# Performance work log

Hardware: AMD Instinct MI355X
Metric: run time of the kernel (lower is better)

The kernel has to match this reference:

```python
import jax, jax.numpy as jnp
import numpy as np

N_HEAD = 12
D_MODEL = 768
D_K = 64
D_V = 64
ALPHA = 1.0
DIST_SCALE = 1.0
TEMPERATURE = D_K ** 0.5
LN_EPS = 1e-6
EPS = 1e-12

B = 16
SEQ = 577  # 1 CLS + 24*24 patches


def setup_inputs() -> dict:
    key = jax.random.key(0)
    ks = jax.random.split(key, 10)
    s = 1.0 / np.sqrt(D_MODEL)
    return {
        "q": jax.random.normal(ks[0], (B, SEQ, D_MODEL), jnp.float32),
        "k": jax.random.normal(ks[1], (B, SEQ, D_MODEL), jnp.float32),
        "v": jax.random.normal(ks[2], (B, SEQ, D_MODEL), jnp.float32),
        "patch_positions": jax.random.uniform(ks[3], (B, SEQ - 1, 2), jnp.float32) * 24.0,
        "patch_embeddings": jax.random.normal(ks[4], (B, SEQ, D_MODEL), jnp.float32),
        # weights stored as (in, out): y = x @ W
        "w_qs": jax.random.normal(ks[5], (D_MODEL, N_HEAD * D_K), jnp.float32) * s,
        "w_ks": jax.random.normal(ks[6], (D_MODEL, N_HEAD * D_K), jnp.float32) * s,
        "w_vs": jax.random.normal(ks[7], (D_MODEL, N_HEAD * D_V), jnp.float32) * s,
        "w_fc": jax.random.normal(ks[8], (N_HEAD * D_V, D_MODEL), jnp.float32) * s,
        "ln_gamma": jnp.ones((D_MODEL,), jnp.float32),
        "ln_beta": jnp.zeros((D_MODEL,), jnp.float32),
    }


def _shape_bias_penalty(pos, emb, alpha, dist_scale):
    # pos: (B, P, 2) patch coordinates; emb: (B, P, E) patch embeddings (no CLS)
    # penalty[b,i,j] = alpha * cos_sim(e_i, e_j) * dist_scale * ||p_i - p_j||
    diff = pos[:, :, None, :] - pos[:, None, :, :]          # (B, P, P, 2)
    dist = jnp.sqrt(jnp.sum(diff * diff, axis=-1) + EPS)    # (B, P, P)
    e = emb * jax.lax.rsqrt(jnp.sum(emb * emb, axis=-1, keepdims=True) + EPS)
    sim = jnp.einsum("bie,bje->bij", e, e)                  # (B, P, P)
    return alpha * sim * (dist_scale * dist)


def reference(q, k, v, patch_positions, patch_embeddings,
              w_qs, w_ks, w_vs, w_fc, ln_gamma, ln_beta):
    b, n, _ = q.shape
    residual = q
    # project and split heads: (B, H, N, Dh)
    qh = (q @ w_qs).reshape(b, n, N_HEAD, D_K).transpose(0, 2, 1, 3)
    kh = (k @ w_ks).reshape(b, n, N_HEAD, D_K).transpose(0, 2, 1, 3)
    vh = (v @ w_vs).reshape(b, n, N_HEAD, D_V).transpose(0, 2, 1, 3)

    logits = jnp.einsum("bhid,bhjd->bhij", qh / TEMPERATURE, kh)  # (B, H, N, N)
    penalty = _shape_bias_penalty(patch_positions, patch_embeddings[:, 1:, :],
                                  ALPHA, DIST_SCALE)              # (B, P, P)
    logits = logits.at[:, :, 1:, 1:].add(-penalty[:, None, :, :])

    attn = jax.nn.softmax(logits, axis=-1)
    out = jnp.einsum("bhij,bhjd->bhid", attn, vh)                 # (B, H, N, Dv)
    out = out.transpose(0, 2, 1, 3).reshape(b, n, N_HEAD * D_V)
    out = out @ w_fc + residual

    mu = jnp.mean(out, axis=-1, keepdims=True)
    var = jnp.mean((out - mu) ** 2, axis=-1, keepdims=True)
    return (out - mu) * jax.lax.rsqrt(var + LN_EPS) * ln_gamma + ln_beta
```

## Files before the change

### kernel.cpp

```cpp
#include <hip/hip_runtime.h>
#include <hip/hip_bf16.h>

#define B_   16
#define SEQ  577
#define P_   576
#define DM   768
#define NH   12
#define DK   64
#define TEMP 8.0f
#define LNEPS 1e-6f
#define EPS_  1e-12f
#define MROWS (B_*SEQ)

typedef __attribute__((ext_vector_type(8))) short short8;
typedef __attribute__((ext_vector_type(4))) float f32x4;

static const size_t PEN_B = 0;
static const size_t QH_B  = 21233664;
static const size_t KH_B  = 35414016;
static const size_t VH_B  = 49594368;
static const size_t VT_B  = 63774720;
static const size_t OBF_B = 79503360;
static const size_t WT_B  = 93683712;
static const size_t RN_B  = 98402304;
static const size_t FC_B  = QH_B;

__device__ __forceinline__ bool bf_flag(const void* gamma) {
    return (((const unsigned int*)gamma)[0] & 0xFFFFu) != 0u;
}
__device__ __forceinline__ float ldf(const void* p, size_t i, bool bf) {
    if (bf) {
        unsigned int w = ((unsigned int)((const unsigned short*)p)[i]) << 16;
        return __uint_as_float(w);
    }
    return ((const float*)p)[i];
}
__device__ __forceinline__ unsigned short f2bu(float x) {
    __hip_bfloat16 h = __float2bfloat16(x);
    return *(unsigned short*)&h;
}

__device__ __forceinline__ int xcd_chunk(int orig, int nwg) {
    int q = nwg >> 3, r = nwg & 7;
    int xcd = orig & 7, slot = orig >> 3;
    int base = xcd < r ? xcd * (q + 1) : r * (q + 1) + (xcd - r) * q;
    return base + slot;
}

__global__ __launch_bounds__(256) void k_rownorm(const void* __restrict__ emb,
                                                 const void* __restrict__ gamma,
                                                 float* __restrict__ rn) {
    bool bf = bf_flag(gamma);
    int row = blockIdx.x;
    int b = row / P_, i = row % P_;
    size_t base = ((size_t)(b * SEQ + 1 + i)) * DM;
    float s = 0.f;
    for (int c = threadIdx.x; c < DM; c += 256) { float v = ldf(emb, base + c, bf); s += v * v; }
    __shared__ float red[4];
    for (int off = 32; off > 0; off >>= 1) s += __shfl_down(s, off, 64);
    int lane = threadIdx.x & 63, w = threadIdx.x >> 6;
    if (lane == 0) red[w] = s;
    __syncthreads();
    if (threadIdx.x == 0) rn[row] = rsqrtf(red[0] + red[1] + red[2] + red[3] + EPS_);
}

__global__ __launch_bounds__(256) void k_wt(const void* __restrict__ w0,
                                            const void* __restrict__ w1,
                                            const void* __restrict__ w2,
                                            const void* __restrict__ w3,
                                            const void* __restrict__ gamma,
                                            unsigned short* __restrict__ wt) {
    bool bf = bf_flag(gamma);
    int which = blockIdx.z;
    const void* W = which == 0 ? w0 : (which == 1 ? w1 : (which == 2 ? w2 : w3));
    unsigned short* WT = wt + (size_t)which * DM * DM;
    int k0 = blockIdx.y * 64, n0 = blockIdx.x * 64;
    __shared__ unsigned short Ts[64][69];
    int tid = threadIdx.x;
    {
        int kr = tid >> 2, nq = (tid & 3) * 16;
        size_t src = (size_t)(k0 + kr) * DM + n0 + nq;
        #pragma unroll
        for (int u = 0; u < 16; u++) Ts[kr][nq + u] = f2bu(ldf(W, src + u, bf));
    }
    __syncthreads();
    {
        int nr = tid >> 2, kq = (tid & 3) * 16;
        unsigned short tmp[16];
        #pragma unroll
        for (int u = 0; u < 16; u++) tmp[u] = Ts[kq + u][nr];
        uint4* dst = (uint4*)(WT + (size_t)(n0 + nr) * DM + k0 + kq);
        dst[0] = *(const uint4*)&tmp[0];
        dst[1] = *(const uint4*)&tmp[8];
    }
}

__global__ __launch_bounds__(256) void k_penalty_mfma(const void* __restrict__ emb,
                                                      const void* __restrict__ pos,
                                                      const void* __restrict__ gamma,
                                                      const float* __restrict__ rn,
                                                      float* __restrict__ pen) {
    bool bf = bf_flag(gamma);
    int p = xcd_chunk(blockIdx.x, 9 * 9 * B_);
    int b = p / 81; int rem = p % 81;
    int i0 = (rem / 9) * 64, j0 = (rem % 9) * 64;
    __shared__ __align__(16) unsigned short As[64][72];
    __shared__ __align__(16) unsigned short Bs[64][72];
    int tid = threadIdx.x;
    int lane = tid & 63, w = tid >> 6;

    f32x4 acc[4];
    #pragma unroll
    for (int c = 0; c < 4; c++) acc[c] = (f32x4){0.f, 0.f, 0.f, 0.f};

    int srow = tid >> 2, sq = (tid & 3) * 16;
    size_t ebase = ((size_t)b * SEQ + 1) * DM;
    size_t sa = ebase + (size_t)(i0 + srow) * DM + sq;
    size_t sb = ebase + (size_t)(j0 + srow) * DM + sq;

    for (int kc = 0; kc < DM; kc += 64) {
        if (bf) {
            const uint4* pa = (const uint4*)((const unsigned short*)emb + sa + kc);
            const uint4* pb = (const uint4*)((const unsigned short*)emb + sb + kc);
            *(uint4*)&As[srow][sq] = pa[0]; *(uint4*)&As[srow][sq + 8] = pa[1];
            *(uint4*)&Bs[srow][sq] = pb[0]; *(uint4*)&Bs[srow][sq + 8] = pb[1];
        } else {
            const float* pa = (const float*)emb + sa + kc;
            const float* pb = (const float*)emb + sb + kc;
            unsigned short ta[16], tb[16];
            #pragma unroll
            for (int u = 0; u < 4; u++) {
                float4 fa = ((const float4*)pa)[u];
                float4 fb = ((const float4*)pb)[u];
                ta[u*4+0] = f2bu(fa.x); ta[u*4+1] = f2bu(fa.y);
                ta[u*4+2] = f2bu(fa.z); ta[u*4+3] = f2bu(fa.w);
                tb[u*4+0] = f2bu(fb.x); tb[u*4+1] = f2bu(fb.y);
                tb[u*4+2] = f2bu(fb.z); tb[u*4+3] = f2bu(fb.w);
            }
            *(uint4*)&As[srow][sq] = *(const uint4*)&ta[0];
            *(uint4*)&As[srow][sq + 8] = *(const uint4*)&ta[8];
            *(uint4*)&Bs[srow][sq] = *(const uint4*)&tb[0];
            *(uint4*)&Bs[srow][sq + 8] = *(const uint4*)&tb[8];
        }
        __syncthreads();
        #pragma unroll
        for (int s = 0; s < 2; s++) {
            short8 af = *(const short8*)&As[w * 16 + (lane & 15)][s * 32 + (lane >> 4) * 8];
            #pragma unroll
            for (int c = 0; c < 4; c++) {
                short8 bfr = *(const short8*)&Bs[c * 16 + (lane & 15)][s * 32 + (lane >> 4) * 8];
                acc[c] = __builtin_amdgcn_mfma_f32_16x16x32_bf16(af, bfr, acc[c], 0, 0, 0);
            }
        }
        __syncthreads();
    }
    size_t pbase = (size_t)b * P_ * 2;
    int rbase = (lane >> 4) * 4, cbase = lane & 15;
    float pix[4], piy[4], rni_[4], pjx[4], pjy[4], rnj_[4];
    #pragma unroll
    for (int jj = 0; jj < 4; jj++) {
        int i = i0 + w * 16 + rbase + jj;
        pix[jj] = ldf(pos, pbase + (size_t)i * 2, bf);
        piy[jj] = ldf(pos, pbase + (size_t)i * 2 + 1, bf);
        rni_[jj] = rn[b * P_ + i];
    }
    #pragma unroll
    for (int c = 0; c < 4; c++) {
        int j = j0 + c * 16 + cbase;
        pjx[c] = ldf(pos, pbase + (size_t)j * 2, bf);
        pjy[c] = ldf(pos, pbase + (size_t)j * 2 + 1, bf);
        rnj_[c] = rn[b * P_ + j];
    }
    float* pp = pen + (size_t)b * P_ * P_;
    #pragma unroll
    for (int c = 0; c < 4; c++)
        #pragma unroll
        for (int jj = 0; jj < 4; jj++) {
            int i = i0 + w * 16 + rbase + jj;
            int j = j0 + c * 16 + cbase;
            float dx = pix[jj] - pjx[c], dy = piy[jj] - pjy[c];
            pp[(size_t)i * P_ + j] = acc[c][jj] * rni_[jj] * rnj_[c] * sqrtf(dx * dx + dy * dy + EPS_);
        }
}

__global__ __launch_bounds__(256) void k_proj_mfma(const void* __restrict__ q,
                                                   const void* __restrict__ k,
                                                   const void* __restrict__ v,
                                                   const unsigned short* __restrict__ wt,
                                                   const void* __restrict__ gamma,
                                                   unsigned short* __restrict__ qh,
                                                   unsigned short* __restrict__ kh,
                                                   unsigned short* __restrict__ vh) {
    bool bf = bf_flag(gamma);
    int p = xcd_chunk(blockIdx.x, 73 * 6 * 3);
    int which = p / (73 * 6);
    int rem = p % (73 * 6);
    int m0 = (rem / 6) * 128, n0 = (rem % 6) * 128;
    const void* X = which == 0 ? q : (which == 1 ? k : v);
    const unsigned short* WT = wt + (size_t)which * DM * DM;
    unsigned short* Y = which == 0 ? qh : (which == 1 ? kh : vh);
    float scale = which == 0 ? (1.0f / TEMP) : 1.0f;

    __shared__ __align__(16) unsigned short As[128][72];
    __shared__ __align__(16) unsigned short Bs[128][72];
    int tid = threadIdx.x;
    int lane = tid & 63, w = tid >> 6;
    int wr = w >> 1, wc = w & 1;

    f32x4 acc[4][4];
    #pragma unroll
    for (int r = 0; r < 4; r++)
        #pragma unroll
        for (int c = 0; c < 4; c++) acc[r][c] = (f32x4){0.f, 0.f, 0.f, 0.f};

    int sr = tid >> 1, sh = (tid & 1) * 32;
    int gm_s = m0 + sr; if (gm_s >= MROWS) gm_s = MROWS - 1;
    const size_t arow = (size_t)gm_s * DM;
    const size_t brow = (size_t)(n0 + sr) * DM;

    for (int kc = 0; kc < DM; kc += 64) {
        if (bf) {
            const uint4* src = (const uint4*)((const unsigned short*)X + arow + kc + sh);
            #pragma unroll
            for (int u = 0; u < 4; u++) *(uint4*)&As[sr][sh + u * 8] = src[u];
        } else {
            const float* src = (const float*)X + arow + kc + sh;
            unsigned short tmp[32];
            #pragma unroll
            for (int u = 0; u < 8; u++) {
                float4 f = ((const float4*)src)[u];
                tmp[u*4+0] = f2bu(f.x); tmp[u*4+1] = f2bu(f.y);
                tmp[u*4+2] = f2bu(f.z); tmp[u*4+3] = f2bu(f.w);
            }
            #pragma unroll
            for (int u = 0; u < 4; u++) *(uint4*)&As[sr][sh + u * 8] = *(const uint4*)&tmp[u * 8];
        }
        {
            const uint4* src = (const uint4*)(WT + brow + kc + sh);
            #pragma unroll
            for (int u = 0; u < 4; u++) *(uint4*)&Bs[sr][sh + u * 8] = src[u];
        }
        __syncthreads();
        #pragma unroll
        for (int s = 0; s < 2; s++) {
            short8 af[4], bfr[4];
            #pragma unroll
            for (int r = 0; r < 4; r++)
                af[r] = *(const short8*)&As[wr * 64 + r * 16 + (lane & 15)][s * 32 + (lane >> 4) * 8];
            #pragma unroll
            for (int c = 0; c < 4; c++)
                bfr[c] = *(const short8*)&Bs[wc * 64 + c * 16 + (lane & 15)][s * 32 + (lane >> 4) * 8];
            #pragma unroll
            for (int r = 0; r < 4; r++)
                #pragma unroll
                for (int c = 0; c < 4; c++)
                    acc[r][c] = __builtin_amdgcn_mfma_f32_16x16x32_bf16(af[r], bfr[c], acc[r][c], 0, 0, 0);
        }
        __syncthreads();
    }
    int rbase = (lane >> 4) * 4, cbase = lane & 15;
    #pragma unroll
    for (int r = 0; r < 4; r++) {
        #pragma unroll
        for (int jj = 0; jj < 4; jj++) {
            int gm = m0 + wr * 64 + r * 16 + rbase + jj;
            if (gm < MROWS) {
                int b = gm / SEQ, n = gm % SEQ;
                #pragma unroll
                for (int c = 0; c < 4; c++) {
                    int gc = n0 + wc * 64 + c * 16 + cbase;
                    int h = gc >> 6, d = gc & 63;
                    Y[(((size_t)(b * NH + h) * SEQ) + n) * DK + d] = f2bu(acc[r][c][jj] * scale);
                }
            }
        }
    }
}

__global__ __launch_bounds__(256) void k_vt(const unsigned short* __restrict__ vh,
                                            unsigned short* __restrict__ vt) {
    int ntile = blockIdx.x;
    int bh = blockIdx.y;
    __shared__ unsigned short Ts[64][72];
    int tid = threadIdx.x;
    int n0 = ntile * 64;
    {
        int r = tid >> 2, c = (tid & 3) * 16;
        int gn = n0 + r; if (gn > 576) gn = 576;
        const uint4* src = (const uint4*)(vh + ((size_t)bh * SEQ + gn) * DK + c);
        uint4 a = src[0], bv = src[1];
        *(uint4*)&Ts[r][c] = a; *(uint4*)&Ts[r][c + 8] = bv;
    }
    __syncthreads();
    {
        int d = tid >> 2, c = (tid & 3) * 16;
        unsigned short tmp[16];
        #pragma unroll
        for (int u = 0; u < 16; u++) tmp[u] = Ts[c + u][d];
        uint4* dst = (uint4*)(vt + ((size_t)bh * DK + d) * 640 + n0 + c);
        dst[0] = *(uint4*)&tmp[0];
        dst[1] = *(uint4*)&tmp[8];
    }
}

__global__ __launch_bounds__(512, 4) void k_attn2(const unsigned short* __restrict__ qh,
                                                  const unsigned short* __restrict__ kh,
                                                  const unsigned short* __restrict__ vt,
                                                  const float* __restrict__ pen,
                                                  unsigned short* __restrict__ O) {
    const int NWG = 5 * NH * B_;
    int flat = blockIdx.x + 5 * (blockIdx.y + NH * blockIdx.z);
    int id = (flat & 7) * (NWG >> 3) + (flat >> 3);
    int it = id % 5; int t2 = id / 5;
    int h = t2 % NH;  int b = t2 / NH;
    int bh = b * NH + h;
    int i0 = it * 128;

    __shared__ __align__(16) unsigned short Qs[128][72];
    __shared__ __align__(16) unsigned short Ks[64][72];
    __shared__ __align__(16) unsigned short Vs[64][72];
    __shared__ __align__(16) unsigned short Ps[128][72];
    int tid = threadIdx.x;
    int lane = tid & 63, w = tid >> 6;

    {
        int r = tid >> 2, c = (tid & 3) * 16;
        int gi = i0 + r; if (gi > 576) gi = 576;
        const uint4* src = (const uint4*)(qh + ((size_t)bh * SEQ + gi) * DK + c);
        uint4 a = src[0], bv = src[1];
        *(uint4*)&Qs[r][c] = a; *(uint4*)&Qs[r][c + 8] = bv;
    }
    __syncthreads();
    short8 qfrag[2];
    #pragma unroll
    for (int s = 0; s < 2; s++)
        qfrag[s] = *(const short8*)&Qs[w * 16 + (lane & 15)][s * 32 + (lane >> 4) * 8];

    f32x4 o_acc[4];
    #pragma unroll
    for (int i = 0; i < 4; i++) o_acc[i] = (f32x4){0.f, 0.f, 0.f, 0.f};
    float m_run[4], l_run[4];
    #pragma unroll
    for (int r = 0; r < 4; r++) { m_run[r] = -1e30f; l_run[r] = 0.f; }

    const float* penb = pen + (size_t)b * P_ * P_;
    int colbase = lane & 15;
    int rloc = (lane >> 4) * 4;

    const float* prow[4]; bool iok[4];
    #pragma unroll
    for (int rg = 0; rg < 4; rg++) {
        int i = i0 + w * 16 + rloc + rg;
        int ii = i < 1 ? 1 : (i > 576 ? 576 : i);
        prow[rg] = penb + (size_t)(ii - 1) * P_;
        iok[rg] = (i >= 1 && i <= 576);
    }

    for (int kt = 0; kt < 10; kt++) {
        int j0 = kt * 64;
        {
            int r = tid >> 3, c = (tid & 7) * 8;
            int gj = j0 + r; if (gj > 576) gj = 576;
            *(uint4*)&Ks[r][c] = *(const uint4*)(kh + ((size_t)bh * SEQ + gj) * DK + c);
            *(uint4*)&Vs[r][c] = *(const uint4*)(vt + ((size_t)bh * DK + r) * 640 + j0 + c);
        }
        __syncthreads();

        float pf[4][4];
        #pragma unroll
        for (int rg = 0; rg < 4; rg++) {
            #pragma unroll
            for (int nt = 0; nt < 4; nt++) {
                int j = j0 + nt * 16 + colbase;
                int jj = j < 1 ? 1 : (j > 576 ? 576 : j);
                float pv = prow[rg][jj - 1];
                pf[rg][nt] = (iok[rg] && j >= 1 && j <= 576) ? pv : 0.f;
            }
        }

        f32x4 sfrag[4];
        __builtin_amdgcn_s_setprio(1);
        #pragma unroll
        for (int nt = 0; nt < 4; nt++) {
            f32x4 acc = (f32x4){0.f, 0.f, 0.f, 0.f};
            #pragma unroll
            for (int s = 0; s < 2; s++) {
                short8 bfrag = *(const short8*)&Ks[nt * 16 + colbase][s * 32 + (lane >> 4) * 8];
                acc = __builtin_amdgcn_mfma_f32_16x16x32_bf16(qfrag[s], bfrag, acc, 0, 0, 0);
            }
            sfrag[nt] = acc;
        }
        __builtin_amdgcn_s_setprio(0);

        #pragma unroll
        for (int nt = 0; nt < 4; nt++) {
            int j = j0 + nt * 16 + colbase;
            #pragma unroll
            for (int rg = 0; rg < 4; rg++) {
                float sv = sfrag[nt][rg] - pf[rg][nt];
                if (j > 576) sv = -1e30f;
                sfrag[nt][rg] = sv;
            }
        }
        float alpha[4];
        #pragma unroll
        for (int rg = 0; rg < 4; rg++) {
            float t = fmaxf(fmaxf(sfrag[0][rg], sfrag[1][rg]),
                            fmaxf(sfrag[2][rg], sfrag[3][rg]));
            #pragma unroll
            for (int off = 1; off < 16; off <<= 1) t = fmaxf(t, __shfl_xor(t, off, 64));
            float mn = fmaxf(m_run[rg], t);
            alpha[rg] = __expf(m_run[rg] - mn);
            m_run[rg] = mn;
        }
        float rsum[4] = {0.f, 0.f, 0.f, 0.f};
        #pragma unroll
        for (int nt = 0; nt < 4; nt++) {
            #pragma unroll
            for (int rg = 0; rg < 4; rg++) {
                float p = __expf(sfrag[nt][rg] - m_run[rg]);
                rsum[rg] += p;
                Ps[w * 16 + rloc + rg][nt * 16 + colbase] = f2bu(p);
            }
        }
        #pragma unroll
        for (int rg = 0; rg < 4; rg++) {
            float t = rsum[rg];
            #pragma unroll
            for (int off = 1; off < 16; off <<= 1) t += __shfl_xor(t, off, 64);
            l_run[rg] = l_run[rg] * alpha[rg] + t;
        }
        #pragma unroll
        for (int nt = 0; nt < 4; nt++)
            #pragma unroll
            for (int rg = 0; rg < 4; rg++) o_acc[nt][rg] *= alpha[rg];

        __builtin_amdgcn_s_setprio(1);
        #pragma unroll
        for (int s = 0; s < 2; s++) {
            short8 afrag = *(const short8*)&Ps[w * 16 + (lane & 15)][s * 32 + (lane >> 4) * 8];
            #pragma unroll
            for (int nt = 0; nt < 4; nt++) {
                short8 bfrag = *(const short8*)&Vs[nt * 16 + colbase][s * 32 + (lane >> 4) * 8];
                o_acc[nt] = __builtin_amdgcn_mfma_f32_16x16x32_bf16(afrag, bfrag, o_acc[nt], 0, 0, 0);
            }
        }
        __builtin_amdgcn_s_setprio(0);
        __syncthreads();
    }
    #pragma unroll
    for (int rg = 0; rg < 4; rg++) {
        int i = i0 + w * 16 + rloc + rg;
        if (i < SEQ) {
            float linv = 1.0f / l_run[rg];
            #pragma unroll
            for (int nt = 0; nt < 4; nt++) {
                int d = nt * 16 + colbase;
                O[(((size_t)(b * SEQ + i)) * NH + h) * DK + d] = f2bu(o_acc[nt][rg] * linv);
            }
        }
    }
}

__global__ __launch_bounds__(256) void k_fc_mfma(const unsigned short* __restrict__ Obf,
                                                 const unsigned short* __restrict__ wtfc,
                                                 const void* __restrict__ qin,
                                                 const void* __restrict__ gamma,
                                                 float* __restrict__ fcout) {
    bool bf = bf_flag(gamma);
    int p = xcd_chunk(blockIdx.x, 73 * 6);
    int m0 = (p / 6) * 128, n0 = (p % 6) * 128;
    __shared__ __align__(16) unsigned short As[128][72];
    __shared__ __align__(16) unsigned short Bs[128][72];
    int tid = threadIdx.x;
    int lane = tid & 63, w = tid >> 6;
    int wr = w >> 1, wc = w & 1;

    f32x4 acc[4][4];
    #pragma unroll
    for (int r = 0; r < 4; r++)
        #pragma unroll
        for (int c = 0; c < 4; c++) acc[r][c] = (f32x4){0.f, 0.f, 0.f, 0.f};

    int sr = tid >> 1, sh = (tid & 1) * 32;
    int gm_s = m0 + sr; if (gm_s >= MROWS) gm_s = MROWS - 1;
    const size_t arow = (size_t)gm_s * DM;
    const size_t brow = (size_t)(n0 + sr) * DM;

    for (int kc = 0; kc < DM; kc += 64) {
        {
            const uint4* src = (const uint4*)(Obf + arow + kc + sh);
            #pragma unroll
            for (int u = 0; u < 4; u++) *(uint4*)&As[sr][sh + u * 8] = src[u];
        }
        {
            const uint4* src = (const uint4*)(wtfc + brow + kc + sh);
            #pragma unroll
            for (int u = 0; u < 4; u++) *(uint4*)&Bs[sr][sh + u * 8] = src[u];
        }
        __syncthreads();
        #pragma unroll
        for (int s = 0; s < 2; s++) {
            short8 af[4], bfr[4];
            #pragma unroll
            for (int r = 0; r < 4; r++)
                af[r] = *(const short8*)&As[wr * 64 + r * 16 + (lane & 15)][s * 32 + (lane >> 4) * 8];
            #pragma unroll
            for (int c = 0; c < 4; c++)
                bfr[c] = *(const short8*)&Bs[wc * 64 + c * 16 + (lane & 15)][s * 32 + (lane >> 4) * 8];
            #pragma unroll
            for (int r = 0; r < 4; r++)
                #pragma unroll
                for (int c = 0; c < 4; c++)
                    acc[r][c] = __builtin_amdgcn_mfma_f32_16x16x32_bf16(af[r], bfr[c], acc[r][c], 0, 0, 0);
        }
        __syncthreads();
    }
    int rbase = (lane >> 4) * 4, cbase = lane & 15;
    #pragma unroll
    for (int r = 0; r < 4; r++) {
        #pragma unroll
        for (int jj = 0; jj < 4; jj++) {
            int gm = m0 + wr * 64 + r * 16 + rbase + jj;
            if (gm < MROWS) {
                #pragma unroll
                for (int c = 0; c < 4; c++) {
                    int gc = n0 + wc * 64 + c * 16 + cbase;
                    fcout[(size_t)gm * DM + gc] = acc[r][c][jj] + ldf(qin, (size_t)gm * DM + gc, bf);
                }
            }
        }
    }
}

__global__ __launch_bounds__(256) void k_ln(const float* __restrict__ x,
                                            const void* __restrict__ gamma,
                                            const void* __restrict__ beta,
                                            void* __restrict__ out) {
    bool bf = bf_flag(gamma);
    int row = blockIdx.x;
    const float* xr = x + (size_t)row * DM;
    int tid = threadIdx.x;
    float v[3];
    float ssum = 0.f;
    #pragma unroll
    for (int u = 0; u < 3; u++) { v[u] = xr[tid + u * 256]; ssum += v[u]; }
    __shared__ float red[4];
    __shared__ float mu_s, var_s;
    float t = ssum;
    for (int off = 32; off > 0; off >>= 1) t += __shfl_down(t, off, 64);
    int lane = tid & 63, w = tid >> 6;
    if (lane == 0) red[w] = t;
    __syncthreads();
    if (tid == 0) mu_s = (red[0] + red[1] + red[2] + red[3]) * (1.0f / DM);
    __syncthreads();
    float mu = mu_s;
    float vs = 0.f;
    #pragma unroll
    for (int u = 0; u < 3; u++) { float d = v[u] - mu; vs += d * d; }
    t = vs;
    for (int off = 32; off > 0; off >>= 1) t += __shfl_down(t, off, 64);
    if (lane == 0) red[w] = t;
    __syncthreads();
    if (tid == 0) var_s = (red[0] + red[1] + red[2] + red[3]) * (1.0f / DM);
    __syncthreads();
    float rstd = rsqrtf(var_s + LNEPS);
    #pragma unroll
    for (int u = 0; u < 3; u++) {
        int c = tid + u * 256;
        float val = (v[u] - mu) * rstd * ldf(gamma, c, bf) + ldf(beta, c, bf);
        size_t idx = (size_t)row * DM + c;
        if (bf) ((__hip_bfloat16*)out)[idx] = __float2bfloat16(val);
        else    ((float*)out)[idx] = val;
    }
}

extern "C" void kernel_launch(void* const* d_in, const int* in_sizes, int n_in,
                              void* d_out, int out_size, void* d_ws, size_t ws_size,
                              hipStream_t stream) {
    const void* q   = d_in[0];
    const void* k   = d_in[1];
    const void* v   = d_in[2];
    const void* pos = d_in[3];
    const void* pe  = d_in[4];
    const void* wq  = d_in[5];
    const void* wk  = d_in[6];
    const void* wv  = d_in[7];
    const void* wfc = d_in[8];
    const void* gam = d_in[9];
    const void* bet = d_in[10];
    char* wsb = (char*)d_ws;
    float*          pen = (float*)(wsb + PEN_B);
    unsigned short* qh  = (unsigned short*)(wsb + QH_B);
    unsigned short* kh  = (unsigned short*)(wsb + KH_B);
    unsigned short* vh  = (unsigned short*)(wsb + VH_B);
    unsigned short* vt  = (unsigned short*)(wsb + VT_B);
    unsigned short* Obf = (unsigned short*)(wsb + OBF_B);
    unsigned short* wt  = (unsigned short*)(wsb + WT_B);
    float*          rn  = (float*)(wsb + RN_B);
    float*          fc  = (float*)(wsb + FC_B);

    k_wt<<<dim3(12, 12, 4), 256, 0, stream>>>(wq, wk, wv, wfc, gam, wt);
    k_rownorm<<<B_ * P_, 256, 0, stream>>>(pe, gam, rn);
    k_penalty_mfma<<<dim3(9 * 9 * B_), 256, 0, stream>>>(pe, pos, gam, rn, pen);
    k_proj_mfma<<<dim3(73 * 6 * 3), 256, 0, stream>>>(q, k, v, wt, gam, qh, kh, vh);
    k_vt<<<dim3(10, 192), 256, 0, stream>>>(vh, vt);
    k_attn2<<<dim3(5, NH, B_), 512, 0, stream>>>(qh, kh, vt, pen, Obf);
    k_fc_mfma<<<dim3(73 * 6), 256, 0, stream>>>(Obf, wt + (size_t)3 * DM * DM, q, gam, fc);
    k_ln<<<MROWS, 256, 0, stream>>>(fc, gam, bet, d_out);
}
```

Before: 438.5 us.

## Stage GEMM tiles via direct global-to-LDS loads and convert fp32 on read

The penalty, projection and FC GEMM kernels now load operand tiles straight from global memory into LDS with the global_load_lds builtin, skipping the register round trip. For fp32 inputs the raw floats are staged in LDS and converted to bf16 when fragments are read (pack8), not before storing. LDS row padding is removed to fit the fixed destination layout of the direct loads. This may bring LDS bank conflicts on fragment reads, doubles LDS footprint for fp32 tiles, and repeats the conversion per fragment read.

```diff
diff --git a/kernel.cpp b/kernel.cpp
--- a/kernel.cpp
+++ b/kernel.cpp
@@ -38,6 +38,21 @@
 __device__ __forceinline__ unsigned short f2bu(float x) {
     __hip_bfloat16 h = __float2bfloat16(x);
     return *(unsigned short*)&h;
+}
+__device__ __forceinline__ short8 pack8(const float* p) {
+    short8 r;
+    #pragma unroll
+    for (int u = 0; u < 8; u++) {
+        __hip_bfloat16 h = __float2bfloat16(p[u]);
+        r[u] = *(short*)&h;
+    }
+    return r;
+}
+__device__ __forceinline__ void gload16(const void* g, void* l) {
+    __builtin_amdgcn_global_load_lds(
+        (const __attribute__((address_space(1))) unsigned int*)g,
+        (__attribute__((address_space(3))) unsigned int*)l,
+        16, 0, 0);
 }
 
 __device__ __forceinline__ int xcd_chunk(int orig, int nwg) {
@@ -104,8 +119,10 @@
     int p = xcd_chunk(blockIdx.x, 9 * 9 * B_);
     int b = p / 81; int rem = p % 81;
     int i0 = (rem / 9) * 64, j0 = (rem % 9) * 64;
-    __shared__ __align__(16) unsigned short As[64][72];
-    __shared__ __align__(16) unsigned short Bs[64][72];
+    __shared__ __align__(16) float Af[64][64];
+    __shared__ __align__(16) float Bf[64][64];
+    unsigned short (*Ab)[64] = (unsigned short(*)[64])Af;
+    unsigned short (*Bb)[64] = (unsigned short(*)[64])Bf;
     int tid = threadIdx.x;
     int lane = tid & 63, w = tid >> 6;
 
@@ -113,42 +130,49 @@
     #pragma unroll
     for (int c = 0; c < 4; c++) acc[c] = (f32x4){0.f, 0.f, 0.f, 0.f};
 
-    int srow = tid >> 2, sq = (tid & 3) * 16;
     size_t ebase = ((size_t)b * SEQ + 1) * DM;
-    size_t sa = ebase + (size_t)(i0 + srow) * DM + sq;
-    size_t sb = ebase + (size_t)(j0 + srow) * DM + sq;
+    const float *aSf[4], *bSf[4]; void *aDf[4], *bDf[4];
+    const unsigned short *aSb[2], *bSb[2]; void *aDb[2], *bDb[2];
+    if (!bf) {
+        #pragma unroll
+        for (int s = 0; s < 4; s++) {
+            int S = w * 4 + s;
+            int ra = i0 + S * 4 + (lane >> 4);
+            int rb = j0 + S * 4 + (lane >> 4);
+            aSf[s] = (const float*)emb + ebase + (size_t)ra * DM + (lane & 15) * 4;
+            bSf[s] = (const float*)emb + ebase + (size_t)rb * DM + (lane & 15) * 4;
+            aDf[s] = &Af[S * 4][0]; bDf[s] = &Bf[S * 4][0];
+        }
+    } else {
+        #pragma unroll
+        for (int s = 0; s < 2; s++) {
+            int S = w * 2 + s;
+            int ra = i0 + S * 8 + (lane >> 3);
+            int rb = j0 + S * 8 + (lane >> 3);
+            aSb[s] = (const unsigned short*)emb + ebase + (size_t)ra * DM + (lane & 7) * 8;
+            bSb[s] = (const unsigned short*)emb + ebase + (size_t)rb * DM + (lane & 7) * 8;
+            aDb[s] = &Ab[S * 8][0]; bDb[s] = &Bb[S * 8][0];
+        }
+    }
 
     for (int kc = 0; kc < DM; kc += 64) {
-        if (bf) {
-            const uint4* pa = (const uint4*)((const unsigned short*)emb + sa + kc);
-            const uint4* pb = (const uint4*)((const unsigned short*)emb + sb + kc);
-            *(uint4*)&As[srow][sq] = pa[0]; *(uint4*)&As[srow][sq + 8] = pa[1];
-            *(uint4*)&Bs[srow][sq] = pb[0]; *(uint4*)&Bs[srow][sq + 8] = pb[1];
+        if (!bf) {
+            #pragma unroll
+            for (int s = 0; s < 4; s++) { gload16(aSf[s] + kc, aDf[s]); gload16(bSf[s] + kc, bDf[s]); }
         } else {
-            const float* pa = (const float*)emb + sa + kc;
-            const float* pb = (const float*)emb + sb + kc;
-            unsigned short ta[16], tb[16];
-            #pragma unroll
-            for (int u = 0; u < 4; u++) {
-                float4 fa = ((const float4*)pa)[u];
-                float4 fb = ((const float4*)pb)[u];
-                ta[u*4+0] = f2bu(fa.x); ta[u*4+1] = f2bu(fa.y);
-                ta[u*4+2] = f2bu(fa.z); ta[u*4+3] = f2bu(fa.w);
-                tb[u*4+0] = f2bu(fb.x); tb[u*4+1] = f2bu(fb.y);
-                tb[u*4+2] = f2bu(fb.z); tb[u*4+3] = f2bu(fb.w);
-            }
-            *(uint4*)&As[srow][sq] = *(const uint4*)&ta[0];
-            *(uint4*)&As[srow][sq + 8] = *(const uint4*)&ta[8];
-            *(uint4*)&Bs[srow][sq] = *(const uint4*)&tb[0];
-            *(uint4*)&Bs[srow][sq + 8] = *(const uint4*)&tb[8];
+            #pragma unroll
+            for (int s = 0; s < 2; s++) { gload16(aSb[s] + kc, aDb[s]); gload16(bSb[s] + kc, bDb[s]); }
         }
         __syncthreads();
         #pragma unroll
         for (int s = 0; s < 2; s++) {
-            short8 af = *(const short8*)&As[w * 16 + (lane & 15)][s * 32 + (lane >> 4) * 8];
+            int co = s * 32 + (lane >> 4) * 8;
+            short8 af = bf ? *(const short8*)&Ab[w * 16 + (lane & 15)][co]
+                           : pack8(&Af[w * 16 + (lane & 15)][co]);
             #pragma unroll
             for (int c = 0; c < 4; c++) {
-                short8 bfr = *(const short8*)&Bs[c * 16 + (lane & 15)][s * 32 + (lane >> 4) * 8];
+                short8 bfr = bf ? *(const short8*)&Bb[c * 16 + (lane & 15)][co]
+                                : pack8(&Bf[c * 16 + (lane & 15)][co]);
                 acc[c] = __builtin_amdgcn_mfma_f32_16x16x32_bf16(af, bfr, acc[c], 0, 0, 0);
             }
         }
@@ -201,8 +225,9 @@
     unsigned short* Y = which == 0 ? qh : (which == 1 ? kh : vh);
     float scale = which == 0 ? (1.0f / TEMP) : 1.0f;
 
-    __shared__ __align__(16) unsigned short As[128][72];
-    __shared__ __align__(16) unsigned short Bs[128][72];
+    __shared__ __align__(16) float Af[128][64];
+    __shared__ __align__(16) unsigned short Bs[128][64];
+    unsigned short (*Ab)[64] = (unsigned short(*)[64])Af;
     int tid = threadIdx.x;
     int lane = tid & 63, w = tid >> 6;
     int wr = w >> 1, wc = w & 1;
@@ -213,43 +238,57 @@
         #pragma unroll
         for (int c = 0; c < 4; c++) acc[r][c] = (f32x4){0.f, 0.f, 0.f, 0.f};
 
-    int sr = tid >> 1, sh = (tid & 1) * 32;
-    int gm_s = m0 + sr; if (gm_s >= MROWS) gm_s = MROWS - 1;
-    const size_t arow = (size_t)gm_s * DM;
-    const size_t brow = (size_t)(n0 + sr) * DM;
+    const float* aSf[8]; void* aDf[8];
+    const unsigned short* aSb[4]; void* aDb[4];
+    const unsigned short* bS[4]; void* bD[4];
+    if (!bf) {
+        #pragma unroll
+        for (int s = 0; s < 8; s++) {
+            int S = w * 8 + s;
+            int row = m0 + S * 4 + (lane >> 4); if (row >= MROWS) row = MROWS - 1;
+            aSf[s] = (const float*)X + (size_t)row * DM + (lane & 15) * 4;
+            aDf[s] = &Af[S * 4][0];
+        }
+    } else {
+        #pragma unroll
+        for (int s = 0; s < 4; s++) {
+            int S = w * 4 + s;
+            int row = m0 + S * 8 + (lane >> 3); if (row >= MROWS) row = MROWS - 1;
+            aSb[s] = (const unsigned short*)X + (size_t)row * DM + (lane & 7) * 8;
+            aDb[s] = &Ab[S * 8][0];
+        }
+    }
+    #pragma unroll
+    for (int s = 0; s < 4; s++) {
+        int S = w * 4 + s;
+        int row = n0 + S * 8 + (lane >> 3);
+        bS[s] = WT + (size_t)row * DM + (lane & 7) * 8;
+        bD[s] = &Bs[S * 8][0];
+    }
 
     for (int kc = 0; kc < DM; kc += 64) {
-        if (bf) {
-            const uint4* src = (const uint4*)((const unsigned short*)X + arow + kc + sh);
-            #pragma unroll
-            for (int u = 0; u < 4; u++) *(uint4*)&As[sr][sh + u * 8] = src[u];
+        if (!bf) {
+            #pragma unroll
+            for (int s = 0; s < 8; s++) gload16(aSf[s] + kc, aDf[s]);
         } else {
-            const float* src = (const float*)X + arow + kc + sh;
-            unsigned short tmp[32];
-            #pragma unroll
-            for (int u = 0; u < 8; u++) {
-                float4 f = ((const float4*)src)[u];
-                tmp[u*4+0] = f2bu(f.x); tmp[u*4+1] = f2bu(f.y);
-                tmp[u*4+2] = f2bu(f.z); tmp[u*4+3] = f2bu(f.w);
-            }
-            #pragma unroll
-            for (int u = 0; u < 4; u++) *(uint4*)&As[sr][sh + u * 8] = *(const uint4*)&tmp[u * 8];
-        }
-        {
-            const uint4* src = (const uint4*)(WT + brow + kc + sh);
-            #pragma unroll
-            for (int u = 0; u < 4; u++) *(uint4*)&Bs[sr][sh + u * 8] = src[u];
-        }
+            #pragma unroll
+            for (int s = 0; s < 4; s++) gload16(aSb[s] + kc, aDb[s]);
+        }
+        #pragma unroll
+        for (int s = 0; s < 4; s++) gload16(bS[s] + kc, bD[s]);
         __syncthreads();
         #pragma unroll
         for (int s = 0; s < 2; s++) {
+            int co = s * 32 + (lane >> 4) * 8;
             short8 af[4], bfr[4];
             #pragma unroll
-            for (int r = 0; r < 4; r++)
-                af[r] = *(const short8*)&As[wr * 64 + r * 16 + (lane & 15)][s * 32 + (lane >> 4) * 8];
+            for (int r = 0; r < 4; r++) {
+                int row = wr * 64 + r * 16 + (lane & 15);
+                af[r] = bf ? *(const short8*)&Ab[row][co] : pack8(&Af[row][co]);
+            }
             #pragma unroll
             for (int c = 0; c < 4; c++)
-                bfr[c] = *(const short8*)&Bs[wc * 64 + c * 16 + (lane & 15)][s * 32 + (lane >> 4) * 8];
+                bfr[c] = *(const short8*)&Bs[wc * 64 + c * 16 + (lane & 15)][co];
             #pragma unroll
             for (int r = 0; r < 4; r++)
                 #pragma unroll
@@ -470,8 +509,8 @@
     bool bf = bf_flag(gamma);
     int p = xcd_chunk(blockIdx.x, 73 * 6);
     int m0 = (p / 6) * 128, n0 = (p % 6) * 128;
-    __shared__ __align__(16) unsigned short As[128][72];
-    __shared__ __align__(16) unsigned short Bs[128][72];
+    __shared__ __align__(16) unsigned short As[128][64];
+    __shared__ __align__(16) unsigned short Bs[128][64];
     int tid = threadIdx.x;
     int lane = tid & 63, w = tid >> 6;
     int wr = w >> 1, wc = w & 1;
@@ -482,32 +521,31 @@
         #pragma unroll
         for (int c = 0; c < 4; c++) acc[r][c] = (f32x4){0.f, 0.f, 0.f, 0.f};
 
-    int sr = tid >> 1, sh = (tid & 1) * 32;
-    int gm_s = m0 + sr; if (gm_s >= MROWS) gm_s = MROWS - 1;
-    const size_t arow = (size_t)gm_s * DM;
-    const size_t brow = (size_t)(n0 + sr) * DM;
+    const unsigned short *aS[4], *bS[4]; void *aD[4], *bD[4];
+    #pragma unroll
+    for (int s = 0; s < 4; s++) {
+        int S = w * 4 + s;
+        int ra = m0 + S * 8 + (lane >> 3); if (ra >= MROWS) ra = MROWS - 1;
+        int rb = n0 + S * 8 + (lane >> 3);
+        aS[s] = Obf + (size_t)ra * DM + (lane & 7) * 8;
+        bS[s] = wtfc + (size_t)rb * DM + (lane & 7) * 8;
+        aD[s] = &As[S * 8][0]; bD[s] = &Bs[S * 8][0];
+    }
 
     for (int kc = 0; kc < DM; kc += 64) {
-        {
-            const uint4* src = (const uint4*)(Obf + arow + kc + sh);
-            #pragma unroll
-            for (int u = 0; u < 4; u++) *(uint4*)&As[sr][sh + u * 8] = src[u];
-        }
-        {
-            const uint4* src = (const uint4*)(wtfc + brow + kc + sh);
-            #pragma unroll
-            for (int u = 0; u < 4; u++) *(uint4*)&Bs[sr][sh + u * 8] = src[u];
-        }
+        #pragma unroll
+        for (int s = 0; s < 4; s++) { gload16(aS[s] + kc, aD[s]); gload16(bS[s] + kc, bD[s]); }
         __syncthreads();
         #pragma unroll
         for (int s = 0; s < 2; s++) {
+            int co = s * 32 + (lane >> 4) * 8;
             short8 af[4], bfr[4];
             #pragma unroll
             for (int r = 0; r < 4; r++)
-                af[r] = *(const short8*)&As[wr * 64 + r * 16 + (lane & 15)][s * 32 + (lane >> 4) * 8];
+                af[r] = *(const short8*)&As[wr * 64 + r * 16 + (lane & 15)][co];
             #pragma unroll
             for (int c = 0; c < 4; c++)
-                bfr[c] = *(const short8*)&Bs[wc * 64 + c * 16 + (lane & 15)][s * 32 + (lane >> 4) * 8];
+                bfr[c] = *(const short8*)&Bs[wc * 64 + c * 16 + (lane & 15)][co];
             #pragma unroll
             for (int r = 0; r < 4; r++)
                 #pragma unroll
```

Measured after the change: 740.1 us. +68.8%, slower.
